# Optimization experiments

Hardware: AMD Instinct MI355X
Metric: run time of the kernel (lower is better)

Reference implementation:

```python
import jax, jax.numpy as jnp
import numpy as np

MB, SEQ, EMBDIM, N_TOKENS = 8, 2048, 64, 8192


def setup_inputs() -> dict:
    key = jax.random.key(0)
    k1, k2 = jax.random.split(key)
    X = jax.random.normal(k1, (MB, SEQ, EMBDIM), dtype=jnp.float32)
    weight = jax.random.normal(k2, (N_TOKENS, EMBDIM), dtype=jnp.float32)
    return {"X": X, "weight": weight}


def reference(X, weight):
    adotb = jnp.einsum("bse,ne->bsn", X, weight)            # [mb, seq, n_tokens]
    adota = jnp.sum(X * X, axis=-1, keepdims=True)           # [mb, seq, 1]
    bdotb = jnp.sum(weight * weight, axis=-1)                # [n_tokens]
    dist = adota - 2.0 * adotb + bdotb                       # [mb, seq, n_tokens]
    return jnp.argmin(dist, axis=-1)                         # [mb, seq] int indices
```

## Files before the change

kernel.cpp:

```cpp
#include <hip/hip_runtime.h>
#include <math.h>

#define EMB     64
#define NTOK    8192
#define NQ      16384
#define TPB     512
#define BQ      256
#define TILE_C  128
#define TCH     (TILE_C * EMB)

typedef _Float16 half8 __attribute__((ext_vector_type(8)));
typedef float    f32x4 __attribute__((ext_vector_type(4)));

__device__ __forceinline__ void gl2lds16(const _Float16* g, _Float16* l) {
    __builtin_amdgcn_global_load_lds(
        (const __attribute__((address_space(1))) unsigned int*)g,
        (__attribute__((address_space(3))) unsigned int*)l, 16, 0, 0);
}

__global__ void prep_kernel(const float* __restrict__ W,
                            _Float16* __restrict__ Wh, _Float16* __restrict__ Wl,
                            float* __restrict__ ynorm) {
    int c = blockIdx.x * blockDim.x + threadIdx.x;
    if (c >= NTOK) return;
    const int g = c >> 4, r = c & 15;
    const float* wp = W + (size_t)c * EMB;
    float s = 0.f;
#pragma unroll
    for (int seg = 0; seg < 8; ++seg) {
        float4 v0 = *(const float4*)(wp + seg * 8);
        float4 v1 = *(const float4*)(wp + seg * 8 + 4);
        float xv[8] = {v0.x, v0.y, v0.z, v0.w, v1.x, v1.y, v1.z, v1.w};
        half8 h, l;
#pragma unroll
        for (int j = 0; j < 8; ++j) {
            _Float16 hh = (_Float16)xv[j];
            h[j] = hh;
            l[j] = (_Float16)(xv[j] - (float)hh);
            s = fmaf(xv[j], xv[j], s);
        }
        const int kb = seg >> 2, lq = seg & 3;
        const size_t u = (size_t)g * 128 + kb * 64 + lq * 16 + r;
        *(half8*)(Wh + u * 8) = h;
        *(half8*)(Wl + u * 8) = l;
    }
    ynorm[c] = s;
}

template <int CS>
__global__ __launch_bounds__(TPB, 2) void vq_mfma_kernel(
    const float* __restrict__ X,
    const _Float16* __restrict__ Wh, const _Float16* __restrict__ Wl,
    const float* __restrict__ ynorm,
    float* __restrict__ pval, int* __restrict__ pidx)
{
    constexpr int CRANGE = NTOK / CS;
    constexpr int NT     = CRANGE / TILE_C;

    __shared__ __align__(16) _Float16 LdsH0[TCH];
    __shared__ __align__(16) _Float16 LdsH1[TCH];
    __shared__ __align__(16) _Float16 LdsL0[TCH];
    __shared__ __align__(16) _Float16 LdsL1[TCH];
    __shared__ __align__(16) float    Lyn[CRANGE];
    __shared__ float RedV[2][BQ];
    __shared__ int   RedI[2][BQ];

    const int t    = threadIdx.x;
    const int lane = t & 63;
    const int wid  = t >> 6;
    const int wq   = wid & 3;
    const int wy   = wid >> 2;
    const int l15  = lane & 15;
    const int lq   = lane >> 4;

    const int qblk   = blockIdx.x * BQ;
    const int qbase  = qblk + wq * 64;
    const int cbase0 = blockIdx.y * CRANGE;

    {
        const size_t gsbase = (size_t)(cbase0 >> 4) * 1024;
#pragma unroll
        for (int i = 0; i < 2; ++i) {
            const int jw = i * 512 + wid * 64;
            gl2lds16(Wh + gsbase + (size_t)(jw + lane) * 8, LdsH0 + (size_t)jw * 8);
            gl2lds16(Wl + gsbase + (size_t)(jw + lane) * 8, LdsL0 + (size_t)jw * 8);
        }
    }

    for (int u = t; u < CRANGE / 4; u += TPB)
        ((float4*)Lyn)[u] = ((const float4*)(ynorm + cbase0))[u];

    half8 ah[4][2], al[4][2];
#pragma unroll
    for (int mt = 0; mt < 4; ++mt) {
#pragma unroll
        for (int kb = 0; kb < 2; ++kb) {
            const float* xp = X + (size_t)(qbase + mt * 16 + l15) * EMB + kb * 32 + lq * 8;
            float4 v0 = *(const float4*)xp;
            float4 v1 = *(const float4*)(xp + 4);
            float xv[8] = {v0.x, v0.y, v0.z, v0.w, v1.x, v1.y, v1.z, v1.w};
            half8 h, l;
#pragma unroll
            for (int j = 0; j < 8; ++j) {
                _Float16 hh = (_Float16)xv[j];
                h[j] = hh;
                l[j] = (_Float16)(xv[j] - (float)hh);
            }
            ah[mt][kb] = h;
            al[mt][kb] = l;
        }
    }

    float minv[4][4];
    int   mini[4][4];
#pragma unroll
    for (int mt = 0; mt < 4; ++mt)
#pragma unroll
        for (int r = 0; r < 4; ++r) { minv[mt][r] = INFINITY; mini[mt][r] = 0; }

    const f32x4 zero4 = {0.f, 0.f, 0.f, 0.f};

    __syncthreads();

    int cur = 0;
    for (int tt = 0; tt < NT; ++tt) {
        if (tt + 1 < NT) {
            const size_t gsbase = (size_t)((cbase0 + (tt + 1) * TILE_C) >> 4) * 1024;
            _Float16* dH = (cur ^ 1) ? LdsH1 : LdsH0;
            _Float16* dL = (cur ^ 1) ? LdsL1 : LdsL0;
#pragma unroll
            for (int i = 0; i < 2; ++i) {
                const int jw = i * 512 + wid * 64;
                gl2lds16(Wh + gsbase + (size_t)(jw + lane) * 8, dH + (size_t)jw * 8);
                gl2lds16(Wl + gsbase + (size_t)(jw + lane) * 8, dL + (size_t)jw * 8);
            }
        }

        const _Float16* LH = cur ? LdsH1 : LdsH0;
        const _Float16* LL = cur ? LdsL1 : LdsL0;
        const int c0 = tt * TILE_C;
#pragma unroll
        for (int ct = 0; ct < 4; ++ct) {
            const int chunk0 = (wy * 4 + ct) * 128 + lane;
            half8 bh0 = *(const half8*)(LH + (size_t)chunk0 * 8);
            half8 bl0 = *(const half8*)(LL + (size_t)chunk0 * 8);
            half8 bh1 = *(const half8*)(LH + (size_t)(chunk0 + 64) * 8);
            half8 bl1 = *(const half8*)(LL + (size_t)(chunk0 + 64) * 8);
            f32x4 acc[4];
#pragma unroll
            for (int mt = 0; mt < 4; ++mt) {
                f32x4 a = __builtin_amdgcn_mfma_f32_16x16x32_f16(al[mt][0], bl0, zero4, 0, 0, 0);
                a = __builtin_amdgcn_mfma_f32_16x16x32_f16(al[mt][0], bh0, a, 0, 0, 0);
                a = __builtin_amdgcn_mfma_f32_16x16x32_f16(ah[mt][0], bl0, a, 0, 0, 0);
                a = __builtin_amdgcn_mfma_f32_16x16x32_f16(ah[mt][0], bh0, a, 0, 0, 0);
                a = __builtin_amdgcn_mfma_f32_16x16x32_f16(al[mt][1], bl1, a, 0, 0, 0);
                a = __builtin_amdgcn_mfma_f32_16x16x32_f16(al[mt][1], bh1, a, 0, 0, 0);
                a = __builtin_amdgcn_mfma_f32_16x16x32_f16(ah[mt][1], bl1, a, 0, 0, 0);
                a = __builtin_amdgcn_mfma_f32_16x16x32_f16(ah[mt][1], bh1, a, 0, 0, 0);
                acc[mt] = a;
            }
            const int   ccol = wy * 64 + ct * 16;
            const float yn   = Lyn[c0 + ccol + l15];
            const int   cidx = cbase0 + c0 + ccol + l15;
#pragma unroll
            for (int mt = 0; mt < 4; ++mt) {
#pragma unroll
                for (int r = 0; r < 4; ++r) {
                    float s = fmaf(-2.f, acc[mt][r], yn);
                    if (s < minv[mt][r]) { minv[mt][r] = s; mini[mt][r] = cidx; }
                }
            }
        }

        asm volatile("s_waitcnt vmcnt(0)" ::: "memory");
        asm volatile("s_waitcnt lgkmcnt(0)" ::: "memory");
        __builtin_amdgcn_s_barrier();
        cur ^= 1;
    }

#pragma unroll
    for (int mt = 0; mt < 4; ++mt) {
#pragma unroll
        for (int r = 0; r < 4; ++r) {
            float v = minv[mt][r];
            int   i = mini[mt][r];
#pragma unroll
            for (int m = 1; m <= 8; m <<= 1) {
                float ov = __shfl_xor(v, m, 64);
                int   oi = __shfl_xor(i, m, 64);
                if (ov < v || (ov == v && oi < i)) { v = ov; i = oi; }
            }
            if (l15 == 0) {
                int qoff = wq * 64 + mt * 16 + lq * 4 + r;
                RedV[wy][qoff] = v;
                RedI[wy][qoff] = i;
            }
        }
    }
    __syncthreads();

    if (t < BQ) {
        float v0 = RedV[0][t]; int i0 = RedI[0][t];
        float v1 = RedV[1][t]; int i1 = RedI[1][t];
        if (v1 < v0 || (v1 == v0 && i1 < i0)) { v0 = v1; i0 = i1; }
        size_t o = (size_t)blockIdx.y * NQ + qblk + t;
        pval[o] = v0;
        pidx[o] = i0;
    }
}

template <int CS>
__global__ void combine_kernel(const float* __restrict__ pval,
                               const int* __restrict__ pidx,
                               int* __restrict__ out)
{
    int q = blockIdx.x * blockDim.x + threadIdx.x;
    if (q >= NQ) return;
    float bv = pval[q];
    int   bi = pidx[q];
#pragma unroll
    for (int s = 1; s < CS; ++s) {
        float v  = pval[(size_t)s * NQ + q];
        int   i2 = pidx[(size_t)s * NQ + q];
        if (v < bv || (v == bv && i2 < bi)) { bv = v; bi = i2; }
    }
    out[q] = bi;
}

extern "C" void kernel_launch(void* const* d_in, const int* in_sizes, int n_in,
                              void* d_out, int out_size, void* d_ws, size_t ws_size,
                              hipStream_t stream) {
    const float* X = (const float*)d_in[0];
    const float* W = (const float*)d_in[1];

    _Float16* Wh    = (_Float16*)d_ws;
    _Float16* Wl    = Wh + (size_t)NTOK * EMB;
    float*    ynorm = (float*)(Wl + (size_t)NTOK * EMB);
    float*    pval  = ynorm + NTOK;
    int*      out   = (int*)d_out;

    prep_kernel<<<NTOK / 256, 256, 0, stream>>>(W, Wh, Wl, ynorm);

    const size_t fixed = 2u * NTOK * EMB * sizeof(_Float16) + NTOK * sizeof(float);
    if (ws_size >= fixed + (size_t)8 * NQ * 8) {
        int* pidx = (int*)(pval + (size_t)8 * NQ);
        dim3 grid(NQ / BQ, 8);
        vq_mfma_kernel<8><<<grid, TPB, 0, stream>>>(X, Wh, Wl, ynorm, pval, pidx);
        combine_kernel<8><<<NQ / 256, 256, 0, stream>>>(pval, pidx, out);
    } else {
        int* pidx = (int*)(pval + (size_t)4 * NQ);
        dim3 grid(NQ / BQ, 4);
        vq_mfma_kernel<4><<<grid, TPB, 0, stream>>>(X, Wh, Wl, ynorm, pval, pidx);
        combine_kernel<4><<<NQ / 256, 256, 0, stream>>>(pval, pidx, out);
    }
}
```

Measured before the change: 131.6 us.

## Fuse combine into main kernel, drop lo*lo MFMAs, reshape blocks for occupancy

```diff
diff --git a/kernel.cpp b/kernel.cpp
--- a/kernel.cpp
+++ b/kernel.cpp
@@ -4,10 +4,14 @@
 #define EMB     64
 #define NTOK    8192
 #define NQ      16384
-#define TPB     512
-#define BQ      256
+#define TPB     256
+#define CSPLIT  4
+#define CRANGE  (NTOK / CSPLIT)
+#define BQ      128
 #define TILE_C  128
+#define NT      (CRANGE / TILE_C)
 #define TCH     (TILE_C * EMB)
+#define NXBLK   (NQ / BQ)
 
 typedef _Float16 half8 __attribute__((ext_vector_type(8)));
 typedef float    f32x4 __attribute__((ext_vector_type(4)));
@@ -47,16 +51,13 @@
     ynorm[c] = s;
 }
 
-template <int CS>
-__global__ __launch_bounds__(TPB, 2) void vq_mfma_kernel(
+__global__ __launch_bounds__(TPB, 3) void vq_mfma_kernel(
     const float* __restrict__ X,
     const _Float16* __restrict__ Wh, const _Float16* __restrict__ Wl,
     const float* __restrict__ ynorm,
-    float* __restrict__ pval, int* __restrict__ pidx)
+    float* __restrict__ pval, int* __restrict__ pidx,
+    int* __restrict__ cnt, int* __restrict__ out)
 {
-    constexpr int CRANGE = NTOK / CS;
-    constexpr int NT     = CRANGE / TILE_C;
-
     __shared__ __align__(16) _Float16 LdsH0[TCH];
     __shared__ __align__(16) _Float16 LdsH1[TCH];
     __shared__ __align__(16) _Float16 LdsL0[TCH];
@@ -64,24 +65,26 @@
     __shared__ __align__(16) float    Lyn[CRANGE];
     __shared__ float RedV[2][BQ];
     __shared__ int   RedI[2][BQ];
+    __shared__ int   fin;
 
     const int t    = threadIdx.x;
     const int lane = t & 63;
     const int wid  = t >> 6;
-    const int wq   = wid & 3;
-    const int wy   = wid >> 2;
+    const int wq   = wid & 1;
+    const int wy   = wid >> 1;
     const int l15  = lane & 15;
     const int lq   = lane >> 4;
 
-    const int qblk   = blockIdx.x * BQ;
+    const int bx     = blockIdx.x;
+    const int qblk   = bx * BQ;
     const int qbase  = qblk + wq * 64;
     const int cbase0 = blockIdx.y * CRANGE;
 
     {
         const size_t gsbase = (size_t)(cbase0 >> 4) * 1024;
 #pragma unroll
-        for (int i = 0; i < 2; ++i) {
-            const int jw = i * 512 + wid * 64;
+        for (int i = 0; i < 4; ++i) {
+            const int jw = i * 256 + wid * 64;
             gl2lds16(Wh + gsbase + (size_t)(jw + lane) * 8, LdsH0 + (size_t)jw * 8);
             gl2lds16(Wl + gsbase + (size_t)(jw + lane) * 8, LdsL0 + (size_t)jw * 8);
         }
@@ -129,8 +132,8 @@
             _Float16* dH = (cur ^ 1) ? LdsH1 : LdsH0;
             _Float16* dL = (cur ^ 1) ? LdsL1 : LdsL0;
 #pragma unroll
-            for (int i = 0; i < 2; ++i) {
-                const int jw = i * 512 + wid * 64;
+            for (int i = 0; i < 4; ++i) {
+                const int jw = i * 256 + wid * 64;
                 gl2lds16(Wh + gsbase + (size_t)(jw + lane) * 8, dH + (size_t)jw * 8);
                 gl2lds16(Wl + gsbase + (size_t)(jw + lane) * 8, dL + (size_t)jw * 8);
             }
@@ -149,11 +152,9 @@
             f32x4 acc[4];
 #pragma unroll
             for (int mt = 0; mt < 4; ++mt) {
-                f32x4 a = __builtin_amdgcn_mfma_f32_16x16x32_f16(al[mt][0], bl0, zero4, 0, 0, 0);
-                a = __builtin_amdgcn_mfma_f32_16x16x32_f16(al[mt][0], bh0, a, 0, 0, 0);
+                f32x4 a = __builtin_amdgcn_mfma_f32_16x16x32_f16(al[mt][0], bh0, zero4, 0, 0, 0);
                 a = __builtin_amdgcn_mfma_f32_16x16x32_f16(ah[mt][0], bl0, a, 0, 0, 0);
                 a = __builtin_amdgcn_mfma_f32_16x16x32_f16(ah[mt][0], bh0, a, 0, 0, 0);
-                a = __builtin_amdgcn_mfma_f32_16x16x32_f16(al[mt][1], bl1, a, 0, 0, 0);
                 a = __builtin_amdgcn_mfma_f32_16x16x32_f16(al[mt][1], bh1, a, 0, 0, 0);
                 a = __builtin_amdgcn_mfma_f32_16x16x32_f16(ah[mt][1], bl1, a, 0, 0, 0);
                 a = __builtin_amdgcn_mfma_f32_16x16x32_f16(ah[mt][1], bh1, a, 0, 0, 0);
@@ -207,24 +208,28 @@
         pval[o] = v0;
         pidx[o] = i0;
     }
-}
-
-template <int CS>
-__global__ void combine_kernel(const float* __restrict__ pval,
-                               const int* __restrict__ pidx,
-                               int* __restrict__ out)
-{
-    int q = blockIdx.x * blockDim.x + threadIdx.x;
-    if (q >= NQ) return;
-    float bv = pval[q];
-    int   bi = pidx[q];
-#pragma unroll
-    for (int s = 1; s < CS; ++s) {
-        float v  = pval[(size_t)s * NQ + q];
-        int   i2 = pidx[(size_t)s * NQ + q];
-        if (v < bv || (v == bv && i2 < bi)) { bv = v; bi = i2; }
-    }
-    out[q] = bi;
+
+    __threadfence();
+    if (t == 0) {
+        int old = atomicAdd(&cnt[bx], 1);
+        fin = (old == CSPLIT - 1);
+    }
+    __syncthreads();
+    if (fin) {
+        __threadfence();
+        if (t < BQ) {
+            const int q = qblk + t;
+            float bv = pval[q];
+            int   bi = pidx[q];
+#pragma unroll
+            for (int s = 1; s < CSPLIT; ++s) {
+                float v  = pval[(size_t)s * NQ + q];
+                int   i2 = pidx[(size_t)s * NQ + q];
+                if (v < bv || (v == bv && i2 < bi)) { bv = v; bi = i2; }
+            }
+            out[q] = bi;
+        }
+    }
 }
 
 extern "C" void kernel_launch(void* const* d_in, const int* in_sizes, int n_in,
@@ -237,20 +242,12 @@
     _Float16* Wl    = Wh + (size_t)NTOK * EMB;
     float*    ynorm = (float*)(Wl + (size_t)NTOK * EMB);
     float*    pval  = ynorm + NTOK;
+    int*      pidx  = (int*)(pval + (size_t)CSPLIT * NQ);
+    int*      cnt   = pidx + (size_t)CSPLIT * NQ;
     int*      out   = (int*)d_out;
 
-    prep_kernel<<<NTOK / 256, 256, 0, stream>>>(W, Wh, Wl, ynorm);
-
-    const size_t fixed = 2u * NTOK * EMB * sizeof(_Float16) + NTOK * sizeof(float);
-    if (ws_size >= fixed + (size_t)8 * NQ * 8) {
-        int* pidx = (int*)(pval + (size_t)8 * NQ);
-        dim3 grid(NQ / BQ, 8);
-        vq_mfma_kernel<8><<<grid, TPB, 0, stream>>>(X, Wh, Wl, ynorm, pval, pidx);
-        combine_kernel<8><<<NQ / 256, 256, 0, stream>>>(pval, pidx, out);
-    } else {
-        int* pidx = (int*)(pval + (size_t)4 * NQ);
-        dim3 grid(NQ / BQ, 4);
-        vq_mfma_kernel<4><<<grid, TPB, 0, stream>>>(X, Wh, Wl, ynorm, pval, pidx);
-        combine_kernel<4><<<NQ / 256, 256, 0, stream>>>(pval, pidx, out);
-    }
-}
+    hipMemsetAsync(cnt, 0, NXBLK * sizeof(int), stream);
+    prep_kernel<<<NTOK / TPB, TPB, 0, stream>>>(W, Wh, Wl, ynorm);
+    dim3 grid(NXBLK, CSPLIT);
+    vq_mfma_kernel<<<grid, TPB, 0, stream>>>(X, Wh, Wl, ynorm, pval, pidx, cnt, out);
+}
```

New measurement: 154.6 us. +17.5%, slower.
